# Kernel tuning notes

Measured on AMD Instinct MI355X. Metric: run time of the kernel, lower is better.

The kernel has to match this reference:

```python
import jax, jax.numpy as jnp
import numpy as np

N = 1024        # nodes
E = 524288      # directed edges
FE_IN, FE = 2, 64   # edge feat in / mid
FC = 128        # candidate (node) feat
L = 3           # EGAT conv layers
NEG_SLOPE = 0.2 # DGL leaky_relu default


def setup_inputs() -> dict:
    key = jax.random.key(0)
    ks = jax.random.split(key, 12)
    s = 0.05
    return {
        "node_feature": jax.random.normal(ks[0], (N, FC), jnp.float32),
        "edge_feature": jax.random.normal(ks[1], (E, FE_IN), jnp.float32),
        "src": jax.random.randint(ks[2], (E,), 0, N, dtype=jnp.int32),
        "dst": jax.random.randint(ks[3], (E,), 0, N, dtype=jnp.int32),
        # input edge linear (bias=True)
        "W_in": jax.random.normal(ks[4], (FE_IN, FE), jnp.float32) * s,
        "b_in": jnp.zeros((FE,), jnp.float32),
        # per-layer EGATConv params (num_heads=1)
        "W_ni": jax.random.normal(ks[5], (L, FC, FE), jnp.float32) * s,
        "W_nj": jax.random.normal(ks[6], (L, FC, FE), jnp.float32) * s,
        "W_fij": jax.random.normal(ks[7], (L, FE, FE), jnp.float32) * s,
        "W_node": jax.random.normal(ks[8], (L, FC, FC), jnp.float32) * s,
        "attn": jax.random.normal(ks[9], (L, FE), jnp.float32) * s,
        "bias_node": jnp.zeros((L, FC), jnp.float32),
    }


def _edge_softmax(e, dst):
    # softmax of edge logits e[E] over incoming edges of each dst node
    m = jax.ops.segment_max(e, dst, num_segments=N)
    ex = jnp.exp(e - m[dst])
    z = jax.ops.segment_sum(ex, dst, num_segments=N)
    return ex / z[dst]


def reference(node_feature, edge_feature, src, dst, W_in, b_in,
              W_ni, W_nj, W_fij, W_node, attn, bias_node):
    node = node_feature                       # [N, FC]
    ef = edge_feature @ W_in + b_in           # [E, FE]
    for l in range(L):
        f_ni = node @ W_ni[l]                 # [N, FE]
        f_nj = node @ W_nj[l]                 # [N, FE]
        # edge messages: gather src/dst projections + edge projection
        f_out = jax.nn.leaky_relu(f_ni[src] + f_nj[dst] + ef @ W_fij[l],
                                  NEG_SLOPE)  # [E, FE]
        e = jnp.einsum('ef,f->e', f_out, attn[l])   # [E]
        a = _edge_softmax(e, dst)                    # [E]
        h = node @ W_node[l] + bias_node[l]          # [N, FC]
        new_node = jax.ops.segment_sum(a[:, None] * h[src], dst,
                                       num_segments=N)  # [N, FC]
        # residual fusion (use_residual=True, num_heads=1 so squeeze is a no-op)
        node = node + new_node
        ef = ef + f_out
    return node
```

## Files before the change

### kernel.cpp

```cpp
#include <hip/hip_runtime.h>

#define N_NODES 1024
#define E_EDGES 524288
#define FE 64
#define FC 128
#define NLAYERS 3

typedef unsigned short u16;
typedef __attribute__((ext_vector_type(8))) short bf16x8;
typedef __attribute__((ext_vector_type(4))) float f32x4;
typedef __attribute__((ext_vector_type(8))) unsigned short u16x8;

__device__ __forceinline__ float bf2f(u16 u) {
    return __uint_as_float(((unsigned)u) << 16);
}
__device__ __forceinline__ u16 f2bf(float f) {
    unsigned x = __float_as_uint(f);
    return (u16)((x + 0x7FFFu + ((x >> 16) & 1u)) >> 16);
}

__global__ __launch_bounds__(256) void setup_kernel(
    const float* __restrict__ node_feature, const float* __restrict__ Wfij,
    u16* __restrict__ Wt,
    const float* __restrict__ Wni, const float* __restrict__ Wnj,
    const float* __restrict__ Wnode, const float* __restrict__ bias,
    u16* __restrict__ fni, u16* __restrict__ fnj,
    float* __restrict__ h, float* __restrict__ S, float* __restrict__ nodeA)
{
    __shared__ float row[FC];
    const int d = blockIdx.x;
    const int t = threadIdx.x;

    reinterpret_cast<float4*>(S + (size_t)d * N_NODES)[t] = make_float4(0.f, 0.f, 0.f, 0.f);

    if (t < FC) {
        const float v = node_feature[d * FC + t];
        nodeA[d * FC + t] = v;
        row[t] = v;
    }
    if (d < (NLAYERS * FE * FE) / 256) {
        const int i = d * 256 + t;
        const int l = i >> 12, rem = i & 4095;
        const int n = rem >> 6, k = rem & 63;
        Wt[(size_t)l * 4096 + n * 64 + k] = f2bf(Wfij[(size_t)l * 4096 + k * 64 + n]);
    }
    __syncthreads();

    if (t < 64) {
        float a = 0.f;
        #pragma unroll 8
        for (int k = 0; k < FC; k++) a = fmaf(row[k], Wni[k * FE + t], a);
        fni[d * FE + t] = f2bf(a);
    } else if (t < 128) {
        const int f = t - 64;
        float a = 0.f;
        #pragma unroll 8
        for (int k = 0; k < FC; k++) a = fmaf(row[k], Wnj[k * FE + f], a);
        fnj[d * FE + f] = f2bf(a);
    } else {
        const int c = t - 128;
        float a = bias[c];
        #pragma unroll 8
        for (int k = 0; k < FC; k++) a = fmaf(row[k], Wnode[k * FC + c], a);
        h[d * FC + c] = a;
    }
}

template <bool FIRST, bool WRITE_EF>
__global__ void edge_mfma_kernel(
    u16* __restrict__ ef,
    const float* __restrict__ x,
    const float* __restrict__ Win,
    const float* __restrict__ bin,
    const u16* __restrict__ Wt,
    const u16* __restrict__ fni, const u16* __restrict__ fnj,
    const int* __restrict__ src, const int* __restrict__ dst,
    const float* __restrict__ attn,
    float* __restrict__ S)
{
    __shared__ __align__(16) u16 stage[4][16][72];
    __shared__ __align__(16) u16 fol[WRITE_EF ? 4 : 1][16][72];

    const int lane = threadIdx.x & 63;
    const int wid  = threadIdx.x >> 6;
    const int l15  = lane & 15;
    const int grp  = lane >> 4;
    const int wbase = blockIdx.x * 64 + wid * 16;

    #pragma unroll
    for (int it = 0; it < 2; it++) {
        const int row = it * 8 + (lane >> 3);
        const int e = wbase + row;
        const int c8 = (lane & 7) * 8;
        const u16x8 a = *reinterpret_cast<const u16x8*>(fni + (size_t)src[e] * FE + c8);
        const u16x8 b = *reinterpret_cast<const u16x8*>(fnj + (size_t)dst[e] * FE + c8);
        u16x8 s;
        #pragma unroll
        for (int j = 0; j < 8; j++) s[j] = f2bf(bf2f(a[j]) + bf2f(b[j]));
        *reinterpret_cast<u16x8*>(&stage[wid][row][c8]) = s;
    }

    bf16x8 afr0, afr1;
    if constexpr (FIRST) {
        const float2 xx = *reinterpret_cast<const float2*>(x + 2 * (size_t)(wbase + l15));
        #pragma unroll
        for (int half = 0; half < 2; half++) {
            const int c0 = half * 32 + grp * 8;
            const float4 wA0 = *reinterpret_cast<const float4*>(Win + c0);
            const float4 wA1 = *reinterpret_cast<const float4*>(Win + c0 + 4);
            const float4 wB0 = *reinterpret_cast<const float4*>(Win + FE + c0);
            const float4 wB1 = *reinterpret_cast<const float4*>(Win + FE + c0 + 4);
            const float4 b0  = *reinterpret_cast<const float4*>(bin + c0);
            const float4 b1  = *reinterpret_cast<const float4*>(bin + c0 + 4);
            bf16x8 fr;
            fr[0] = (short)f2bf(fmaf(xx.x, wA0.x, fmaf(xx.y, wB0.x, b0.x)));
            fr[1] = (short)f2bf(fmaf(xx.x, wA0.y, fmaf(xx.y, wB0.y, b0.y)));
            fr[2] = (short)f2bf(fmaf(xx.x, wA0.z, fmaf(xx.y, wB0.z, b0.z)));
            fr[3] = (short)f2bf(fmaf(xx.x, wA0.w, fmaf(xx.y, wB0.w, b0.w)));
            fr[4] = (short)f2bf(fmaf(xx.x, wA1.x, fmaf(xx.y, wB1.x, b1.x)));
            fr[5] = (short)f2bf(fmaf(xx.x, wA1.y, fmaf(xx.y, wB1.y, b1.y)));
            fr[6] = (short)f2bf(fmaf(xx.x, wA1.z, fmaf(xx.y, wB1.z, b1.z)));
            fr[7] = (short)f2bf(fmaf(xx.x, wA1.w, fmaf(xx.y, wB1.w, b1.w)));
            if (half == 0) afr0 = fr; else afr1 = fr;
        }
    } else {
        const size_t arow = (size_t)(wbase + l15) * FE;
        afr0 = *reinterpret_cast<const bf16x8*>(ef + arow + grp * 8);
        afr1 = *reinterpret_cast<const bf16x8*>(ef + arow + 32 + grp * 8);
    }

    bf16x8 bfr[2][4];
    #pragma unroll
    for (int ks = 0; ks < 2; ks++)
        #pragma unroll
        for (int nt = 0; nt < 4; nt++)
            bfr[ks][nt] = *reinterpret_cast<const bf16x8*>(
                Wt + (size_t)(nt * 16 + l15) * 64 + ks * 32 + grp * 8);

    f32x4 acc[4];
    #pragma unroll
    for (int nt = 0; nt < 4; nt++) {
        acc[nt] = (f32x4){0.f, 0.f, 0.f, 0.f};
        acc[nt] = __builtin_amdgcn_mfma_f32_16x16x32_bf16(afr0, bfr[0][nt], acc[nt], 0, 0, 0);
        acc[nt] = __builtin_amdgcn_mfma_f32_16x16x32_bf16(afr1, bfr[1][nt], acc[nt], 0, 0, 0);
    }

    float an[4];
    #pragma unroll
    for (int nt = 0; nt < 4; nt++) an[nt] = attn[nt * 16 + l15];

    __builtin_amdgcn_wave_barrier();

    float logit[4] = {0.f, 0.f, 0.f, 0.f};
    #pragma unroll
    for (int nt = 0; nt < 4; nt++) {
        const int n = nt * 16 + l15;
        #pragma unroll
        for (int r = 0; r < 4; r++) {
            const int row = grp * 4 + r;
            float v = acc[nt][r] + bf2f(stage[wid][row][n]);
            v = fmaxf(v, 0.2f * v);
            logit[r] = fmaf(v, an[nt], logit[r]);
            if constexpr (WRITE_EF) fol[wid][row][n] = f2bf(v);
        }
    }

    #pragma unroll
    for (int r = 0; r < 4; r++) {
        float t = logit[r];
        t += __shfl_xor(t, 1, 16);
        t += __shfl_xor(t, 2, 16);
        t += __shfl_xor(t, 4, 16);
        t += __shfl_xor(t, 8, 16);
        if (l15 == 0) {
            const int e = wbase + grp * 4 + r;
            atomicAdd(S + (size_t)dst[e] * N_NODES + src[e], expf(t));
        }
    }

    if constexpr (WRITE_EF) {
        __builtin_amdgcn_wave_barrier();
        const u16x8 fo0 = *reinterpret_cast<const u16x8*>(&fol[wid][l15][grp * 8]);
        const u16x8 fo1 = *reinterpret_cast<const u16x8*>(&fol[wid][l15][32 + grp * 8]);
        u16x8 o0, o1;
        #pragma unroll
        for (int j = 0; j < 8; j++) {
            o0[j] = f2bf(bf2f((u16)afr0[j]) + bf2f(fo0[j]));
            o1[j] = f2bf(bf2f((u16)afr1[j]) + bf2f(fo1[j]));
        }
        u16* gp = ef + (size_t)(wbase + l15) * FE;
        *reinterpret_cast<u16x8*>(gp + grp * 8) = o0;
        *reinterpret_cast<u16x8*>(gp + 32 + grp * 8) = o1;
    }
}

template <bool LAST>
__global__ __launch_bounds__(256) void spmm_kernel(
    float* __restrict__ S, const float* __restrict__ h,
    const float* __restrict__ nin, float* __restrict__ nout,
    const float* __restrict__ Wni, const float* __restrict__ Wnj,
    const float* __restrict__ Wnode, const float* __restrict__ bias,
    u16* __restrict__ fni, u16* __restrict__ fnj, float* __restrict__ hnext)
{
    __shared__ float red[256];
    __shared__ float rs[2];
    __shared__ float row[FC];
    const int d = blockIdx.x;
    const int t = threadIdx.x;
    const int c = t & 127;
    const int half = t >> 7;
    const float* Srow = S + (size_t)d * N_NODES + half * 512;
    const float* hp = h + (size_t)half * 512 * FC;
    float acc = 0.f, rsum = 0.f;
    #pragma unroll 8
    for (int n = 0; n < 512; n++) {
        const float s = Srow[n];
        rsum += s;
        acc = fmaf(s, hp[n * FC + c], acc);
    }
    red[t] = acc;
    if (c == 0) rs[half] = rsum;
    __syncthreads();

    if constexpr (!LAST) {
        reinterpret_cast<float4*>(S + (size_t)d * N_NODES)[t] = make_float4(0.f, 0.f, 0.f, 0.f);
    }
    if (half == 0) {
        const float v = nin[d * FC + c] + (red[c] + red[128 + c]) / (rs[0] + rs[1]);
        nout[d * FC + c] = v;
        if constexpr (!LAST) row[c] = v;
    }

    if constexpr (!LAST) {
        __syncthreads();
        if (t < 64) {
            float a = 0.f;
            #pragma unroll 8
            for (int k = 0; k < FC; k++) a = fmaf(row[k], Wni[k * FE + t], a);
            fni[d * FE + t] = f2bf(a);
        } else if (t < 128) {
            const int f = t - 64;
            float a = 0.f;
            #pragma unroll 8
            for (int k = 0; k < FC; k++) a = fmaf(row[k], Wnj[k * FE + f], a);
            fnj[d * FE + f] = f2bf(a);
        } else {
            const int cc = t - 128;
            float a = bias[cc];
            #pragma unroll 8
            for (int k = 0; k < FC; k++) a = fmaf(row[k], Wnode[k * FC + cc], a);
            hnext[d * FC + cc] = a;
        }
    }
}

extern "C" void kernel_launch(void* const* d_in, const int* in_sizes, int n_in,
                              void* d_out, int out_size, void* d_ws, size_t ws_size,
                              hipStream_t stream)
{
    const float* node_feature = (const float*)d_in[0];
    const float* edge_feature = (const float*)d_in[1];
    const int*   src          = (const int*)d_in[2];
    const int*   dst          = (const int*)d_in[3];
    const float* W_in         = (const float*)d_in[4];
    const float* b_in         = (const float*)d_in[5];
    const float* W_ni         = (const float*)d_in[6];
    const float* W_nj         = (const float*)d_in[7];
    const float* W_fij        = (const float*)d_in[8];
    const float* W_node       = (const float*)d_in[9];
    const float* attn         = (const float*)d_in[10];
    const float* bias_node    = (const float*)d_in[11];
    float* out = (float*)d_out;

    char* ws = (char*)d_ws;
    size_t off = 0;
    auto alloc = [&](size_t bytes) -> void* {
        void* pp = ws + off;
        off += (bytes + 255) & ~(size_t)255;
        return pp;
    };
    u16*   ef    = (u16*)alloc((size_t)E_EDGES * FE * sizeof(u16));
    u16*   fni   = (u16*)alloc(N_NODES * FE * sizeof(u16));
    u16*   fnj   = (u16*)alloc(N_NODES * FE * sizeof(u16));
    float* h0    = (float*)alloc(N_NODES * FC * sizeof(float));
    float* h1    = (float*)alloc(N_NODES * FC * sizeof(float));
    float* S     = (float*)alloc((size_t)N_NODES * N_NODES * sizeof(float));
    float* nodeA = (float*)alloc(N_NODES * FC * sizeof(float));
    u16*   Wt    = (u16*)alloc((size_t)NLAYERS * FE * FE * sizeof(u16));
    float* hbuf[2] = {h0, h1};

    setup_kernel<<<N_NODES, 256, 0, stream>>>(
        node_feature, W_fij, Wt, W_ni, W_nj, W_node, bias_node,
        fni, fnj, h0, S, nodeA);

    for (int l = 0; l < NLAYERS; l++) {
        float* hl = hbuf[l & 1];
        float* hn = hbuf[(l + 1) & 1];

        if (l == 0) {
            edge_mfma_kernel<true, true><<<E_EDGES / 64, 256, 0, stream>>>(
                ef, edge_feature, W_in, b_in, Wt + (size_t)l * FE * FE,
                fni, fnj, src, dst, attn + (size_t)l * FE, S);
        } else if (l == NLAYERS - 1) {
            edge_mfma_kernel<false, false><<<E_EDGES / 64, 256, 0, stream>>>(
                ef, nullptr, nullptr, nullptr, Wt + (size_t)l * FE * FE,
                fni, fnj, src, dst, attn + (size_t)l * FE, S);
        } else {
            edge_mfma_kernel<false, true><<<E_EDGES / 64, 256, 0, stream>>>(
                ef, nullptr, nullptr, nullptr, Wt + (size_t)l * FE * FE,
                fni, fnj, src, dst, attn + (size_t)l * FE, S);
        }

        if (l == NLAYERS - 1) {
            spmm_kernel<true><<<N_NODES, 256, 0, stream>>>(
                S, hl, nodeA, out,
                nullptr, nullptr, nullptr, nullptr, nullptr, nullptr, nullptr);
        } else {
            const int ln = l + 1;
            spmm_kernel<false><<<N_NODES, 256, 0, stream>>>(
                S, hl, nodeA, nodeA,
                W_ni + (size_t)ln * FC * FE, W_nj + (size_t)ln * FC * FE,
                W_node + (size_t)ln * FC * FC, bias_node + (size_t)ln * FC,
                fni, fnj, hn);
        }
    }
}
```

Baseline: 283.9 us.

## Use packed bf16 convert, 32-bit indexing, exp2, and split accumulators

```diff
diff --git a/kernel.cpp b/kernel.cpp
--- a/kernel.cpp
+++ b/kernel.cpp
@@ -7,16 +7,22 @@
 #define NLAYERS 3
 
 typedef unsigned short u16;
+typedef unsigned int u32;
 typedef __attribute__((ext_vector_type(8))) short bf16x8;
 typedef __attribute__((ext_vector_type(4))) float f32x4;
 typedef __attribute__((ext_vector_type(8))) unsigned short u16x8;
+typedef __attribute__((ext_vector_type(4))) unsigned int u32x4;
 
 __device__ __forceinline__ float bf2f(u16 u) {
-    return __uint_as_float(((unsigned)u) << 16);
+    return __uint_as_float(((u32)u) << 16);
+}
+__device__ __forceinline__ u32 cvt2bf(float lo, float hi) {
+    u32 r;
+    asm("v_cvt_pk_bf16_f32 %0, %1, %2" : "=v"(r) : "v"(lo), "v"(hi));
+    return r;
 }
 __device__ __forceinline__ u16 f2bf(float f) {
-    unsigned x = __float_as_uint(f);
-    return (u16)((x + 0x7FFFu + ((x >> 16) & 1u)) >> 16);
+    return (u16)cvt2bf(f, 0.f);
 }
 
 __global__ __launch_bounds__(256) void setup_kernel(
@@ -42,27 +48,36 @@
         const int i = d * 256 + t;
         const int l = i >> 12, rem = i & 4095;
         const int n = rem >> 6, k = rem & 63;
-        Wt[(size_t)l * 4096 + n * 64 + k] = f2bf(Wfij[(size_t)l * 4096 + k * 64 + n]);
+        Wt[(u32)(l * 4096 + n * 64 + k)] = f2bf(Wfij[(u32)(l * 4096 + k * 64 + n)]);
     }
     __syncthreads();
 
     if (t < 64) {
-        float a = 0.f;
+        float a0 = 0.f, a1 = 0.f;
         #pragma unroll 8
-        for (int k = 0; k < FC; k++) a = fmaf(row[k], Wni[k * FE + t], a);
-        fni[d * FE + t] = f2bf(a);
+        for (int k = 0; k < FC; k += 2) {
+            a0 = fmaf(row[k],     Wni[k * FE + t], a0);
+            a1 = fmaf(row[k + 1], Wni[(k + 1) * FE + t], a1);
+        }
+        fni[d * FE + t] = f2bf(a0 + a1);
     } else if (t < 128) {
         const int f = t - 64;
-        float a = 0.f;
+        float a0 = 0.f, a1 = 0.f;
         #pragma unroll 8
-        for (int k = 0; k < FC; k++) a = fmaf(row[k], Wnj[k * FE + f], a);
-        fnj[d * FE + f] = f2bf(a);
+        for (int k = 0; k < FC; k += 2) {
+            a0 = fmaf(row[k],     Wnj[k * FE + f], a0);
+            a1 = fmaf(row[k + 1], Wnj[(k + 1) * FE + f], a1);
+        }
+        fnj[d * FE + f] = f2bf(a0 + a1);
     } else {
         const int c = t - 128;
-        float a = bias[c];
+        float a0 = bias[c], a1 = 0.f;
         #pragma unroll 8
-        for (int k = 0; k < FC; k++) a = fmaf(row[k], Wnode[k * FC + c], a);
-        h[d * FC + c] = a;
+        for (int k = 0; k < FC; k += 2) {
+            a0 = fmaf(row[k],     Wnode[k * FC + c], a0);
+            a1 = fmaf(row[k + 1], Wnode[(k + 1) * FC + c], a1);
+        }
+        h[d * FC + c] = a0 + a1;
     }
 }
 
@@ -92,17 +107,20 @@
         const int row = it * 8 + (lane >> 3);
         const int e = wbase + row;
         const int c8 = (lane & 7) * 8;
-        const u16x8 a = *reinterpret_cast<const u16x8*>(fni + (size_t)src[e] * FE + c8);
-        const u16x8 b = *reinterpret_cast<const u16x8*>(fnj + (size_t)dst[e] * FE + c8);
-        u16x8 s;
-        #pragma unroll
-        for (int j = 0; j < 8; j++) s[j] = f2bf(bf2f(a[j]) + bf2f(b[j]));
-        *reinterpret_cast<u16x8*>(&stage[wid][row][c8]) = s;
+        const u16x8 a = *reinterpret_cast<const u16x8*>(fni + (u32)(src[e] * FE + c8));
+        const u16x8 b = *reinterpret_cast<const u16x8*>(fnj + (u32)(dst[e] * FE + c8));
+        u32x4 s;
+        #pragma unroll
+        for (int j = 0; j < 4; j++) {
+            s[j] = cvt2bf(bf2f(a[2*j]) + bf2f(b[2*j]),
+                          bf2f(a[2*j+1]) + bf2f(b[2*j+1]));
+        }
+        *reinterpret_cast<u32x4*>(&stage[wid][row][c8]) = s;
     }
 
     bf16x8 afr0, afr1;
     if constexpr (FIRST) {
-        const float2 xx = *reinterpret_cast<const float2*>(x + 2 * (size_t)(wbase + l15));
+        const float2 xx = *reinterpret_cast<const float2*>(x + 2 * (u32)(wbase + l15));
         #pragma unroll
         for (int half = 0; half < 2; half++) {
             const int c0 = half * 32 + grp * 8;
@@ -112,19 +130,19 @@
             const float4 wB1 = *reinterpret_cast<const float4*>(Win + FE + c0 + 4);
             const float4 b0  = *reinterpret_cast<const float4*>(bin + c0);
             const float4 b1  = *reinterpret_cast<const float4*>(bin + c0 + 4);
-            bf16x8 fr;
-            fr[0] = (short)f2bf(fmaf(xx.x, wA0.x, fmaf(xx.y, wB0.x, b0.x)));
-            fr[1] = (short)f2bf(fmaf(xx.x, wA0.y, fmaf(xx.y, wB0.y, b0.y)));
-            fr[2] = (short)f2bf(fmaf(xx.x, wA0.z, fmaf(xx.y, wB0.z, b0.z)));
-            fr[3] = (short)f2bf(fmaf(xx.x, wA0.w, fmaf(xx.y, wB0.w, b0.w)));
-            fr[4] = (short)f2bf(fmaf(xx.x, wA1.x, fmaf(xx.y, wB1.x, b1.x)));
-            fr[5] = (short)f2bf(fmaf(xx.x, wA1.y, fmaf(xx.y, wB1.y, b1.y)));
-            fr[6] = (short)f2bf(fmaf(xx.x, wA1.z, fmaf(xx.y, wB1.z, b1.z)));
-            fr[7] = (short)f2bf(fmaf(xx.x, wA1.w, fmaf(xx.y, wB1.w, b1.w)));
-            if (half == 0) afr0 = fr; else afr1 = fr;
+            u32x4 fr;
+            fr[0] = cvt2bf(fmaf(xx.x, wA0.x, fmaf(xx.y, wB0.x, b0.x)),
+                           fmaf(xx.x, wA0.y, fmaf(xx.y, wB0.y, b0.y)));
+            fr[1] = cvt2bf(fmaf(xx.x, wA0.z, fmaf(xx.y, wB0.z, b0.z)),
+                           fmaf(xx.x, wA0.w, fmaf(xx.y, wB0.w, b0.w)));
+            fr[2] = cvt2bf(fmaf(xx.x, wA1.x, fmaf(xx.y, wB1.x, b1.x)),
+                           fmaf(xx.x, wA1.y, fmaf(xx.y, wB1.y, b1.y)));
+            fr[3] = cvt2bf(fmaf(xx.x, wA1.z, fmaf(xx.y, wB1.z, b1.z)),
+                           fmaf(xx.x, wA1.w, fmaf(xx.y, wB1.w, b1.w)));
+            if (half == 0) afr0 = (bf16x8)fr; else afr1 = (bf16x8)fr;
         }
     } else {
-        const size_t arow = (size_t)(wbase + l15) * FE;
+        const u32 arow = (u32)(wbase + l15) * FE;
         afr0 = *reinterpret_cast<const bf16x8*>(ef + arow + grp * 8);
         afr1 = *reinterpret_cast<const bf16x8*>(ef + arow + 32 + grp * 8);
     }
@@ -135,7 +153,7 @@
         #pragma unroll
         for (int nt = 0; nt < 4; nt++)
             bfr[ks][nt] = *reinterpret_cast<const bf16x8*>(
-                Wt + (size_t)(nt * 16 + l15) * 64 + ks * 32 + grp * 8);
+                Wt + (u32)((nt * 16 + l15) * 64 + ks * 32 + grp * 8));
 
     f32x4 acc[4];
     #pragma unroll
@@ -147,7 +165,7 @@
 
     float an[4];
     #pragma unroll
-    for (int nt = 0; nt < 4; nt++) an[nt] = attn[nt * 16 + l15];
+    for (int nt = 0; nt < 4; nt++) an[nt] = attn[nt * 16 + l15] * 1.44269504088896f;
 
     __builtin_amdgcn_wave_barrier();
 
@@ -174,7 +192,7 @@
         t += __shfl_xor(t, 8, 16);
         if (l15 == 0) {
             const int e = wbase + grp * 4 + r;
-            atomicAdd(S + (size_t)dst[e] * N_NODES + src[e], expf(t));
+            atomicAdd(S + (u32)(dst[e] * N_NODES + src[e]), exp2f(t));
         }
     }
 
@@ -182,15 +200,17 @@
         __builtin_amdgcn_wave_barrier();
         const u16x8 fo0 = *reinterpret_cast<const u16x8*>(&fol[wid][l15][grp * 8]);
         const u16x8 fo1 = *reinterpret_cast<const u16x8*>(&fol[wid][l15][32 + grp * 8]);
-        u16x8 o0, o1;
-        #pragma unroll
-        for (int j = 0; j < 8; j++) {
-            o0[j] = f2bf(bf2f((u16)afr0[j]) + bf2f(fo0[j]));
-            o1[j] = f2bf(bf2f((u16)afr1[j]) + bf2f(fo1[j]));
-        }
-        u16* gp = ef + (size_t)(wbase + l15) * FE;
-        *reinterpret_cast<u16x8*>(gp + grp * 8) = o0;
-        *reinterpret_cast<u16x8*>(gp + 32 + grp * 8) = o1;
+        u32x4 o0, o1;
+        #pragma unroll
+        for (int j = 0; j < 4; j++) {
+            o0[j] = cvt2bf(bf2f((u16)afr0[2*j])   + bf2f(fo0[2*j]),
+                           bf2f((u16)afr0[2*j+1]) + bf2f(fo0[2*j+1]));
+            o1[j] = cvt2bf(bf2f((u16)afr1[2*j])   + bf2f(fo1[2*j]),
+                           bf2f((u16)afr1[2*j+1]) + bf2f(fo1[2*j+1]));
+        }
+        u16* gp = ef + (u32)(wbase + l15) * FE;
+        *reinterpret_cast<u32x4*>(gp + grp * 8) = o0;
+        *reinterpret_cast<u32x4*>(gp + 32 + grp * 8) = o1;
     }
 }
 
@@ -211,15 +231,19 @@
     const int half = t >> 7;
     const float* Srow = S + (size_t)d * N_NODES + half * 512;
     const float* hp = h + (size_t)half * 512 * FC;
-    float acc = 0.f, rsum = 0.f;
-    #pragma unroll 8
-    for (int n = 0; n < 512; n++) {
-        const float s = Srow[n];
-        rsum += s;
-        acc = fmaf(s, hp[n * FC + c], acc);
-    }
-    red[t] = acc;
-    if (c == 0) rs[half] = rsum;
+    float a0 = 0.f, a1 = 0.f, a2 = 0.f, a3 = 0.f;
+    float r0 = 0.f, r1 = 0.f, r2 = 0.f, r3 = 0.f;
+    #pragma unroll 4
+    for (int n = 0; n < 512; n += 4) {
+        const float s0 = Srow[n], s1 = Srow[n+1], s2 = Srow[n+2], s3 = Srow[n+3];
+        r0 += s0; r1 += s1; r2 += s2; r3 += s3;
+        a0 = fmaf(s0, hp[n * FC + c], a0);
+        a1 = fmaf(s1, hp[(n+1) * FC + c], a1);
+        a2 = fmaf(s2, hp[(n+2) * FC + c], a2);
+        a3 = fmaf(s3, hp[(n+3) * FC + c], a3);
+    }
+    red[t] = (a0 + a1) + (a2 + a3);
+    if (c == 0) rs[half] = (r0 + r1) + (r2 + r3);
     __syncthreads();
 
     if constexpr (!LAST) {
@@ -234,22 +258,31 @@
     if constexpr (!LAST) {
         __syncthreads();
         if (t < 64) {
-            float a = 0.f;
+            float b0 = 0.f, b1 = 0.f;
             #pragma unroll 8
-            for (int k = 0; k < FC; k++) a = fmaf(row[k], Wni[k * FE + t], a);
-            fni[d * FE + t] = f2bf(a);
+            for (int k = 0; k < FC; k += 2) {
+                b0 = fmaf(row[k],     Wni[k * FE + t], b0);
+                b1 = fmaf(row[k + 1], Wni[(k + 1) * FE + t], b1);
+            }
+            fni[d * FE + t] = f2bf(b0 + b1);
         } else if (t < 128) {
             const int f = t - 64;
-            float a = 0.f;
+            float b0 = 0.f, b1 = 0.f;
             #pragma unroll 8
-            for (int k = 0; k < FC; k++) a = fmaf(row[k], Wnj[k * FE + f], a);
-            fnj[d * FE + f] = f2bf(a);
+            for (int k = 0; k < FC; k += 2) {
+                b0 = fmaf(row[k],     Wnj[k * FE + f], b0);
+                b1 = fmaf(row[k + 1], Wnj[(k + 1) * FE + f], b1);
+            }
+            fnj[d * FE + f] = f2bf(b0 + b1);
         } else {
             const int cc = t - 128;
-            float a = bias[cc];
+            float b0 = bias[cc], b1 = 0.f;
             #pragma unroll 8
-            for (int k = 0; k < FC; k++) a = fmaf(row[k], Wnode[k * FC + cc], a);
-            hnext[d * FC + cc] = a;
+            for (int k = 0; k < FC; k += 2) {
+                b0 = fmaf(row[k],     Wnode[k * FC + cc], b0);
+                b1 = fmaf(row[k + 1], Wnode[(k + 1) * FC + cc], b1);
+            }
+            hnext[d * FC + cc] = b0 + b1;
         }
     }
 }
```

Result: no change. 280.0 us (-1.4%).
